# Kernel tuning notes

Hardware: AMD Instinct MI355X
Metric: run time of the kernel (lower is better)

## Reference

```python
import jax, jax.numpy as jnp
import numpy as np


def conv1x1(x, W, b):
    # x: [B,C,H,W], W: [O,C], b: [O]
    return jnp.einsum('bchw,oc->bohw', x, W) + b[None, :, None, None]


def setup_inputs() -> dict:
    key = jax.random.key(0)
    ks = jax.random.split(key, 16)
    B, C, H, W = 4, 256, 64, 64
    C4 = C // 4
    s = lambda fan_in: 1.0 / np.sqrt(fan_in)
    inp = {
        'last_frame': jax.random.normal(ks[0], (B, C, H, W), jnp.float32),
        'current_frame': jax.random.normal(ks[1], (B, C, H, W), jnp.float32),
        'future_frame': jax.random.normal(ks[2], (B, C, H, W), jnp.float32),
        'Wqk': jax.random.normal(ks[3], (C4, C), jnp.float32) * s(C),
        'bqk': jnp.zeros((C4,), jnp.float32),
        'Wkl': jax.random.normal(ks[4], (C4, C), jnp.float32) * s(C),
        'bkl': jnp.zeros((C4,), jnp.float32),
        'Wkf': jax.random.normal(ks[5], (C4, C), jnp.float32) * s(C),
        'bkf': jnp.zeros((C4,), jnp.float32),
        'Wv': jax.random.normal(ks[6], (C4, C), jnp.float32) * s(C),
        'bv': jnp.zeros((C4,), jnp.float32),
        'Wfire': jax.random.normal(ks[7], (C, C // 2), jnp.float32) * s(C // 2),
        'bfire': jnp.zeros((C,), jnp.float32),
        'bn_gamma': jnp.ones((C,), jnp.float32),
        'bn_beta': jnp.zeros((C,), jnp.float32),
        'bn_mean': jnp.zeros((C,), jnp.float32),
        'bn_var': jnp.ones((C,), jnp.float32),
    }
    return inp


def reference(last_frame, current_frame, future_frame,
              Wqk, bqk, Wkl, bkl, Wkf, bkf, Wv, bv,
              Wfire, bfire, bn_gamma, bn_beta, bn_mean, bn_var):
    B, C, H, W = current_frame.shape
    C4 = C // 4
    HW = H * W
    eps = 1e-5

    q = conv1x1(current_frame, Wqk, bqk).reshape(B, C4, HW)       # [B,C4,HW]
    kl = conv1x1(last_frame, Wkl, bkl).reshape(B, C4, HW)          # [B,C4,HW]
    kf = conv1x1(future_frame, Wkf, bkf).reshape(B, C4, HW)        # [B,C4,HW]
    v = conv1x1(current_frame, Wv, bv).reshape(B, C4, HW)          # [B,C4,HW]

    # affinity: [B, HW(query), HW(key)], softmax over key axis
    aff_l = jax.nn.softmax(jnp.einsum('bcq,bck->bqk', q, kl), axis=-1)
    aff_f = jax.nn.softmax(jnp.einsum('bcq,bck->bqk', q, kf), axis=-1)

    # out = V @ A^T : out[b,c,q] = sum_k v[b,c,k] * aff[b,q,k]
    out_l = jnp.einsum('bck,bqk->bcq', v, aff_l).reshape(B, C4, H, W)
    out_f = jnp.einsum('bck,bqk->bcq', v, aff_f).reshape(B, C4, H, W)

    fused = jnp.concatenate([out_l, out_f], axis=1)                 # [B,C/2,H,W]
    fired = conv1x1(fused, Wfire, bfire)                            # [B,C,H,W]
    # BatchNorm (inference form with running stats)
    inv = bn_gamma / jnp.sqrt(bn_var + eps)
    fired = fired * inv[None, :, None, None] + (bn_beta - bn_mean * inv)[None, :, None, None]
    return jax.nn.relu(current_frame + fired)
```

## Files before the change

### kernel.cpp

```cpp
#include <hip/hip_runtime.h>
#include <math.h>
#include <stdint.h>

#define HWN 4096
#define CIN 256
#define CQ 64
#define LOG2E 1.44269504f
#define C2OFF 56.0f

typedef __attribute__((ext_vector_type(8))) _Float16 f16x8;
typedef __attribute__((ext_vector_type(4))) _Float16 f16x4;
typedef __attribute__((ext_vector_type(8))) short    bf16x8;
typedef __attribute__((ext_vector_type(4))) short    bf16x4;
typedef __attribute__((ext_vector_type(4))) float    f32x4;

__device__ __forceinline__ short f2bf(float f) {
  union { float f; uint32_t u; } c; c.f = f;
  uint32_t r = (c.u + 0x7FFFu + ((c.u >> 16) & 1u)) >> 16;
  return (short)(uint16_t)r;
}

__device__ __forceinline__ void stage16(const void* g, void* l) {
  __builtin_amdgcn_global_load_lds(
      (const __attribute__((address_space(1))) uint32_t*)g,
      (__attribute__((address_space(3))) uint32_t*)l, 16, 0, 0);
}

__device__ __forceinline__ void pswap32(uint32_t& a, uint32_t& b) {
  asm volatile("v_permlane32_swap_b32 %0, %1" : "+v"(a), "+v"(b));
}
__device__ __forceinline__ void pswap16(uint32_t& a, uint32_t& b) {
  asm volatile("v_permlane16_swap_b32 %0, %1" : "+v"(a), "+v"(b));
}

__global__ __launch_bounds__(256) void prep_kernel(
    const float* __restrict__ Wqk, const float* __restrict__ Wkl,
    const float* __restrict__ Wkf, const float* __restrict__ Wv,
    const float* __restrict__ Wfire, const float* __restrict__ bfire,
    const float* __restrict__ gamma, const float* __restrict__ beta,
    const float* __restrict__ mean,  const float* __restrict__ var,
    _Float16* __restrict__ wqk_h, _Float16* __restrict__ wkl_h,
    _Float16* __restrict__ wkf_h, _Float16* __restrict__ wv_h,
    _Float16* __restrict__ wf_h, float* __restrict__ scale, float* __restrict__ shift) {
  int gid = blockIdx.x * 256 + threadIdx.x;
  if (gid < CQ * CIN) {
    wqk_h[gid] = (_Float16)(Wqk[gid] * LOG2E);
    wkl_h[gid] = (_Float16)Wkl[gid];
    wkf_h[gid] = (_Float16)Wkf[gid];
    wv_h[gid]  = (_Float16)Wv[gid];
  }
  if (gid < CIN * 128) wf_h[gid] = (_Float16)Wfire[gid];
  if (gid < CIN) {
    float inv = gamma[gid] / sqrtf(var[gid] + 1e-5f);
    scale[gid] = inv;
    shift[gid] = (bfire[gid] - mean[gid]) * inv + beta[gid];
  }
}

__global__ __launch_bounds__(256, 3) void proj_kernel(
    const float* __restrict__ cur, const float* __restrict__ last, const float* __restrict__ fut,
    const _Float16* __restrict__ wqk, const float* __restrict__ bqk,
    const _Float16* __restrict__ wkl, const float* __restrict__ bkl,
    const _Float16* __restrict__ wkf, const float* __restrict__ bkf,
    const _Float16* __restrict__ wv,  const float* __restrict__ bv,
    _Float16* __restrict__ q_out, _Float16* __restrict__ kl_out,
    _Float16* __restrict__ kf_out, short* __restrict__ v_out) {
  const int tid  = threadIdx.x;
  const int w    = tid >> 6;
  const int lane = tid & 63;
  const int quad = lane >> 4;
  const int l15  = lane & 15;
  const int pass = blockIdx.x >> 8;
  const int bb   = blockIdx.x & 255;
  const int b    = bb >> 6;
  const int hwt  = (bb & 63) << 6;
  const int hw   = hwt + w * 16 + l15;

  __shared__ __align__(16) float    Xs[2][8][260];
  __shared__ __align__(16) _Float16 Tl[4][16][72];

  const float* X = (pass == 0) ? cur : ((pass == 1) ? last : fut);
  const float* xb0 = X + (size_t)b * CIN * HWN + hwt;

  auto stageX = [&](int buf, int cc) {
#pragma unroll
    for (int i = 0; i < 2; ++i)
      stage16(xb0 + (size_t)(cc * 32 + w * 8 + i * 4 + (lane >> 3) / 2) * HWN +
                  ((lane & 15) << 2),
              &Xs[buf][w * 2 + i][0]);
  };

  const _Float16* W1 = (pass == 0) ? wqk : ((pass == 1) ? wkl : wkf);
  f32x4 a1[4] = {};
  f32x4 a2[4] = {};

  stageX(0, 0);
  __syncthreads();
#pragma unroll 1
  for (int cc = 0; cc < 8; ++cc) {
    const int buf = cc & 1;
    if (cc + 1 < 8) stageX(buf ^ 1, cc + 1);
    f16x8 bh;
#pragma unroll
    for (int j = 0; j < 8; ++j) {
      const int g = quad * 2 + (j >> 2);
      bh[j] = (_Float16)Xs[buf][g][(j & 3) * 64 + w * 16 + l15];
    }
#pragma unroll
    for (int mt = 0; mt < 4; ++mt) {
      f16x8 wa = *(const f16x8*)(W1 + (mt * 16 + l15) * CIN + cc * 32 + quad * 8);
      a1[mt] = __builtin_amdgcn_mfma_f32_16x16x32_f16(wa, bh, a1[mt], 0, 0, 0);
    }
    if (pass == 0) {
#pragma unroll
      for (int mt = 0; mt < 4; ++mt) {
        f16x8 wb = *(const f16x8*)(wv + (mt * 16 + l15) * CIN + cc * 32 + quad * 8);
        a2[mt] = __builtin_amdgcn_mfma_f32_16x16x32_f16(wb, bh, a2[mt], 0, 0, 0);
      }
    }
    __syncthreads();
  }

  if (pass == 0) {
#pragma unroll
    for (int mt = 0; mt < 4; ++mt)
#pragma unroll
      for (int r = 0; r < 4; ++r) {
        int oc = mt * 16 + quad * 4 + r;
        q_out[((size_t)b * CQ + oc) * HWN + hw] = (_Float16)(a1[mt][r] + bqk[oc] * LOG2E);
        v_out[((size_t)b * CQ + oc) * HWN + hw] = f2bf(a2[mt][r] + bv[oc]);
      }
  } else {
    const float* BI = (pass == 1) ? bkl : bkf;
    _Float16* OUT = (pass == 1) ? kl_out : kf_out;
#pragma unroll
    for (int mt = 0; mt < 4; ++mt) {
      f16x4 pw;
#pragma unroll
      for (int r = 0; r < 4; ++r)
        pw[r] = (_Float16)(a1[mt][r] + BI[mt * 16 + quad * 4 + r]);
      *(f16x4*)&Tl[w][l15][mt * 16 + quad * 4] = pw;
    }
#pragma unroll
    for (int kk = 0; kk < 2; ++kk) {
      f16x8 row = *(const f16x8*)&Tl[w][l15][kk * 32 + quad * 8];
      *(f16x8*)(OUT + ((size_t)b * HWN + hw) * CQ + kk * 32 + quad * 8) = row;
    }
  }
}

__global__ __launch_bounds__(256, 2) void attn_kernel(
    const _Float16* __restrict__ qbuf, const _Float16* __restrict__ klbuf,
    const _Float16* __restrict__ kfbuf, const short* __restrict__ vbuf,
    _Float16* __restrict__ fused) {
  const int tid  = threadIdx.x;
  const int w    = tid >> 6;
  const int lane = tid & 63;
  const int quad = lane >> 4;
  const int l15  = lane & 15;

  const int xcd  = blockIdx.x & 7;
  const int L    = xcd * 64 + (blockIdx.x >> 3);
  const int qt   = (L & 63) << 6;
  const int pair = (L >> 6) & 1;
  const int b    = L >> 7;

  const int kh = w >> 1;
  const int wq = w & 1;

  const _Float16* K  = (pair ? kfbuf : klbuf) + (size_t)b * HWN * CQ;
  const short*    Vg = vbuf + (size_t)b * CQ * HWN;

  __shared__ __align__(16) _Float16 Kt[2][2][64][64];
  __shared__ __align__(16) short    Vt[2][2][64][64];

  const int qbase = qt + wq * 32;
  f16x8 qfrag[2][2];
#pragma unroll
  for (int qg = 0; qg < 2; ++qg)
#pragma unroll
    for (int kk = 0; kk < 2; ++kk)
#pragma unroll
      for (int j = 0; j < 8; ++j)
        qfrag[qg][kk][j] = qbuf[(b * CQ + kk * 32 + quad * 8 + j) * HWN +
                                qbase + qg * 16 + l15];

  f32x4 Oacc[2][4] = {};
  float psum[2] = {0.f, 0.f};

  const int swz  = (lane & 7) ^ ((lane >> 3) & 7);
  const int rswz = l15 & 7;

  const _Float16* ksrc =
      K + ((size_t)(kh * 2048) + wq * 32 + (lane >> 3)) * CQ + swz * 8;
  const short* vsrcS =
      Vg + (size_t)(wq * 32 + (lane >> 3)) * HWN + kh * 2048 + swz * 8;

  auto stageK = [&](int buf, int t) {
#pragma unroll
    for (int r = 0; r < 4; ++r)
      stage16(ksrc + ((size_t)t * 64 + r * 8) * CQ,
              &Kt[buf][kh][wq * 32 + r * 8][0]);
  };
  auto stageV = [&](int buf, int t) {
#pragma unroll
    for (int r = 0; r < 4; ++r)
      stage16(vsrcS + (size_t)(r * 8) * HWN + t * 64,
              &Vt[buf][kh][wq * 32 + r * 8][0]);
  };

  auto body = [&](int buf) {
    f16x8 kf[4][2];
#pragma unroll
    for (int nt = 0; nt < 4; ++nt)
#pragma unroll
      for (int kk = 0; kk < 2; ++kk)
        kf[nt][kk] = *(const f16x8*)&Kt[buf][kh][nt * 16 + l15][((kk * 4 + quad) ^ rswz) * 8];
    bf16x8 vf[4][2];
#pragma unroll
    for (int ct = 0; ct < 4; ++ct)
#pragma unroll
      for (int kk = 0; kk < 2; ++kk)
        vf[ct][kk] = *(const bf16x8*)&Vt[buf][kh][ct * 16 + l15][((kk * 4 + quad) ^ rswz) * 8];
#pragma unroll
    for (int qg = 0; qg < 2; ++qg) {
      f32x4 ST[4] = {};
      __builtin_amdgcn_s_setprio(1);
#pragma unroll
      for (int nt = 0; nt < 4; ++nt)
#pragma unroll
        for (int kk = 0; kk < 2; ++kk)
          ST[nt] = __builtin_amdgcn_mfma_f32_16x16x32_f16(kf[nt][kk], qfrag[qg][kk],
                                                          ST[nt], 0, 0, 0);
      __builtin_amdgcn_s_setprio(0);
      uint32_t D[4][2];
#pragma unroll
      for (int nt = 0; nt < 4; ++nt)
#pragma unroll
        for (int e = 0; e < 2; ++e) {
          float p0 = __builtin_amdgcn_exp2f(ST[nt][2 * e]     - C2OFF);
          float p1 = __builtin_amdgcn_exp2f(ST[nt][2 * e + 1] - C2OFF);
          uint32_t u0 = __float_as_uint(p0) & 0xffff0000u;
          uint32_t u1 = __float_as_uint(p1) & 0xffff0000u;
          psum[qg] += __uint_as_float(u0) + __uint_as_float(u1);
          D[nt][e] = (u0 >> 16) | u1;
        }
#pragma unroll
      for (int kk = 0; kk < 2; ++kk) {
        uint32_t pa0, pa1, pa2, pa3;
        {
          uint32_t u = D[2 * kk][0], v = D[2 * kk + 1][0];
          pswap32(u, v); pswap16(u, v);
          pa0 = u; pa2 = v;
        }
        {
          uint32_t u = D[2 * kk][1], v = D[2 * kk + 1][1];
          pswap32(u, v); pswap16(u, v);
          pa1 = u; pa3 = v;
        }
        union { uint32_t u[4]; bf16x8 v8; } P;
        P.u[0] = pa0; P.u[1] = pa1; P.u[2] = pa2; P.u[3] = pa3;
        __builtin_amdgcn_s_setprio(1);
#pragma unroll
        for (int ct = 0; ct < 4; ++ct)
          Oacc[qg][ct] = __builtin_amdgcn_mfma_f32_16x16x32_bf16(P.v8, vf[ct][kk],
                                                                 Oacc[qg][ct], 0, 0, 0);
        __builtin_amdgcn_s_setprio(0);
      }
    }
  };

  stageK(0, 0); stageV(0, 0);
  __syncthreads();
#pragma unroll 1
  for (int tt = 0; tt < 32; tt += 2) {
    stageK(1, tt + 1); stageV(1, tt + 1);
    body(0);
    __syncthreads();
    if (tt + 2 < 32) { stageK(0, tt + 2); stageV(0, tt + 2); }
    body(1);
    __syncthreads();
  }

#pragma unroll
  for (int qg = 0; qg < 2; ++qg) {
    psum[qg] += __shfl_xor(psum[qg], 16);
    psum[qg] += __shfl_xor(psum[qg], 32);
  }

  float* sc = (float*)&Kt[0][0][0][0];
  float* sp = sc + 4096;
  if (kh) {
#pragma unroll
    for (int qg = 0; qg < 2; ++qg) {
#pragma unroll
      for (int ct = 0; ct < 4; ++ct)
        *(f32x4*)&sc[((((wq * 2 + qg) * 4) + ct) << 8) + lane * 4] = Oacc[qg][ct];
      sp[(wq * 2 + qg) * 64 + lane] = psum[qg];
    }
  }
  __syncthreads();
  if (!kh) {
#pragma unroll
    for (int qg = 0; qg < 2; ++qg) {
      psum[qg] += sp[(wq * 2 + qg) * 64 + lane];
#pragma unroll
      for (int ct = 0; ct < 4; ++ct) {
        f32x4 o2 = *(const f32x4*)&sc[((((wq * 2 + qg) * 4) + ct) << 8) + lane * 4];
        Oacc[qg][ct] += o2;
      }
#pragma unroll
      for (int r = 0; r < 4; ++r) {
        float lt = __shfl(psum[qg], quad * 4 + r);
        float invl = __builtin_amdgcn_rcpf(lt);
        int qi = qbase + qg * 16 + quad * 4 + r;
#pragma unroll
        for (int ct = 0; ct < 4; ++ct)
          fused[((size_t)b * HWN + qi) * 128 + pair * 64 + ct * 16 + l15] =
              (_Float16)(Oacc[qg][ct][r] * invl);
      }
    }
  }
}

__global__ __launch_bounds__(256) void fire_kernel(
    const _Float16* __restrict__ fused, const _Float16* __restrict__ wf,
    const float* __restrict__ scale, const float* __restrict__ shift,
    const float* __restrict__ cur, float* __restrict__ out) {
  const int tid  = threadIdx.x;
  const int w    = tid >> 6;
  const int lane = tid & 63;
  const int quad = lane >> 4;
  const int l15  = lane & 15;
  const int g    = blockIdx.x & 3;
  const int bb   = blockIdx.x >> 2;
  const int b    = bb >> 6;
  const int hwt  = (bb & 63) << 6;
  const int hwb  = hwt + w * 16;

  f16x8 bfr[4];
#pragma unroll
  for (int k0 = 0; k0 < 4; ++k0)
    bfr[k0] = *(const f16x8*)(fused + ((size_t)b * HWN + hwb + l15) * 128 + k0 * 32 + quad * 8);

  float curv[4][4];
#pragma unroll
  for (int mt = 0; mt < 4; ++mt)
#pragma unroll
    for (int r = 0; r < 4; ++r)
      curv[mt][r] = cur[((size_t)b * CIN + g * 64 + mt * 16 + quad * 4 + r) * HWN + hwb + l15];

  f32x4 acc[4] = {};
#pragma unroll
  for (int k0 = 0; k0 < 4; ++k0)
#pragma unroll
    for (int mt = 0; mt < 4; ++mt) {
      f16x8 af = *(const f16x8*)(wf + (g * 64 + mt * 16 + l15) * 128 + k0 * 32 + quad * 8);
      acc[mt] = __builtin_amdgcn_mfma_f32_16x16x32_f16(af, bfr[k0], acc[mt], 0, 0, 0);
    }

#pragma unroll
  for (int mt = 0; mt < 4; ++mt)
#pragma unroll
    for (int r = 0; r < 4; ++r) {
      int oc = g * 64 + mt * 16 + quad * 4 + r;
      size_t idx = ((size_t)b * CIN + oc) * HWN + hwb + l15;
      float y = curv[mt][r] + acc[mt][r] * scale[oc] + shift[oc];
      out[idx] = fmaxf(y, 0.f);
    }
}

extern "C" void kernel_launch(void* const* d_in, const int* in_sizes, int n_in,
                              void* d_out, int out_size, void* d_ws, size_t ws_size,
                              hipStream_t stream) {
  const float* last  = (const float*)d_in[0];
  const float* cur   = (const float*)d_in[1];
  const float* fut   = (const float*)d_in[2];
  const float* Wqk   = (const float*)d_in[3];
  const float* bqk   = (const float*)d_in[4];
  const float* Wkl   = (const float*)d_in[5];
  const float* bkl   = (const float*)d_in[6];
  const float* Wkf   = (const float*)d_in[7];
  const float* bkf   = (const float*)d_in[8];
  const float* Wv    = (const float*)d_in[9];
  const float* bv    = (const float*)d_in[10];
  const float* Wfire = (const float*)d_in[11];
  const float* bfire = (const float*)d_in[12];
  const float* gamma = (const float*)d_in[13];
  const float* beta  = (const float*)d_in[14];
  const float* mean  = (const float*)d_in[15];
  const float* var   = (const float*)d_in[16];

  char* ws = (char*)d_ws;
  _Float16* qb     = (_Float16*)(ws);
  _Float16* klb    = (_Float16*)(ws + (2u << 20));
  _Float16* kfb    = (_Float16*)(ws + (4u << 20));
  short*    vb     = (short*)   (ws + (6u << 20));
  _Float16* fusedb = (_Float16*)(ws + (8u << 20));
  char* wsm = ws + (12u << 20);
  _Float16* wqk_h = (_Float16*)(wsm);
  _Float16* wkl_h = (_Float16*)(wsm + (32u << 10));
  _Float16* wkf_h = (_Float16*)(wsm + (64u << 10));
  _Float16* wv_h  = (_Float16*)(wsm + (96u << 10));
  _Float16* wf_h  = (_Float16*)(wsm + (128u << 10));
  float*    scale = (float*)   (wsm + (192u << 10));
  float*    shift = (float*)   (wsm + (193u << 10));
  float*    out   = (float*)d_out;

  prep_kernel<<<128, 256, 0, stream>>>(Wqk, Wkl, Wkf, Wv, Wfire, bfire,
                                       gamma, beta, mean, var,
                                       wqk_h, wkl_h, wkf_h, wv_h, wf_h, scale, shift);
  proj_kernel<<<768, 256, 0, stream>>>(cur, last, fut, wqk_h, bqk, wkl_h, bkl,
                                       wkf_h, bkf, wv_h, bv, qb, klb, kfb, vb);
  attn_kernel<<<512, 256, 0, stream>>>(qb, klb, kfb, vb, fusedb);
  fire_kernel<<<1024, 256, 0, stream>>>(fusedb, wf_h, scale, shift, cur, out);
}
```

Measured before the change: 194.9 us.

## Compute softmax row sums via MFMA with ones vector and packed bf16 convert

Replaces per-element bf16 truncation and scalar accumulation of the softmax denominator with a hardware packed f32-to-bf16 conversion, and computes row sums by an extra MFMA of P against a vector of ones. This removes VALU adds and the cross-lane shuffles at the end, at the cost of one more MFMA per kk step and round-to-nearest instead of truncation. The fire kernel also remaps block indices so that consecutive logical tiles land on the same XCD, for better L2 locality.

```diff
diff --git a/kernel.cpp b/kernel.cpp
--- a/kernel.cpp
+++ b/kernel.cpp
@@ -186,7 +186,11 @@
                                 qbase + qg * 16 + l15];
 
   f32x4 Oacc[2][4] = {};
-  float psum[2] = {0.f, 0.f};
+  f32x4 Osum[2]    = {};
+
+  bf16x8 vones;
+#pragma unroll
+  for (int j = 0; j < 8; ++j) vones[j] = (short)0x3F80;
 
   const int swz  = (lane & 7) ^ ((lane >> 3) & 7);
   const int rswz = l15 & 7;
@@ -240,10 +244,8 @@
         for (int e = 0; e < 2; ++e) {
           float p0 = __builtin_amdgcn_exp2f(ST[nt][2 * e]     - C2OFF);
           float p1 = __builtin_amdgcn_exp2f(ST[nt][2 * e + 1] - C2OFF);
-          uint32_t u0 = __float_as_uint(p0) & 0xffff0000u;
-          uint32_t u1 = __float_as_uint(p1) & 0xffff0000u;
-          psum[qg] += __uint_as_float(u0) + __uint_as_float(u1);
-          D[nt][e] = (u0 >> 16) | u1;
+          asm("v_cvt_pk_bf16_f32 %0, %1, %2"
+              : "=v"(D[nt][e]) : "v"(p0), "v"(p1));
         }
 #pragma unroll
       for (int kk = 0; kk < 2; ++kk) {
@@ -265,6 +267,8 @@
         for (int ct = 0; ct < 4; ++ct)
           Oacc[qg][ct] = __builtin_amdgcn_mfma_f32_16x16x32_bf16(P.v8, vf[ct][kk],
                                                                  Oacc[qg][ct], 0, 0, 0);
+        Osum[qg] = __builtin_amdgcn_mfma_f32_16x16x32_bf16(P.v8, vones,
+                                                           Osum[qg], 0, 0, 0);
         __builtin_amdgcn_s_setprio(0);
       }
     }
@@ -282,28 +286,22 @@
     __syncthreads();
   }
 
-#pragma unroll
-  for (int qg = 0; qg < 2; ++qg) {
-    psum[qg] += __shfl_xor(psum[qg], 16);
-    psum[qg] += __shfl_xor(psum[qg], 32);
-  }
-
   float* sc = (float*)&Kt[0][0][0][0];
-  float* sp = sc + 4096;
+  f32x4* sv = (f32x4*)(sc + 4096);
   if (kh) {
 #pragma unroll
     for (int qg = 0; qg < 2; ++qg) {
 #pragma unroll
       for (int ct = 0; ct < 4; ++ct)
         *(f32x4*)&sc[((((wq * 2 + qg) * 4) + ct) << 8) + lane * 4] = Oacc[qg][ct];
-      sp[(wq * 2 + qg) * 64 + lane] = psum[qg];
+      sv[(wq * 2 + qg) * 64 + lane] = Osum[qg];
     }
   }
   __syncthreads();
   if (!kh) {
 #pragma unroll
     for (int qg = 0; qg < 2; ++qg) {
-      psum[qg] += sp[(wq * 2 + qg) * 64 + lane];
+      Osum[qg] += sv[(wq * 2 + qg) * 64 + lane];
 #pragma unroll
       for (int ct = 0; ct < 4; ++ct) {
         f32x4 o2 = *(const f32x4*)&sc[((((wq * 2 + qg) * 4) + ct) << 8) + lane * 4];
@@ -311,8 +309,7 @@
       }
 #pragma unroll
       for (int r = 0; r < 4; ++r) {
-        float lt = __shfl(psum[qg], quad * 4 + r);
-        float invl = __builtin_amdgcn_rcpf(lt);
+        float invl = __builtin_amdgcn_rcpf(Osum[qg][r]);
         int qi = qbase + qg * 16 + quad * 4 + r;
 #pragma unroll
         for (int ct = 0; ct < 4; ++ct)
@@ -332,8 +329,10 @@
   const int lane = tid & 63;
   const int quad = lane >> 4;
   const int l15  = lane & 15;
-  const int g    = blockIdx.x & 3;
-  const int bb   = blockIdx.x >> 2;
+  const int xcd  = blockIdx.x & 7;
+  const int Lf   = xcd * 128 + (blockIdx.x >> 3);
+  const int g    = Lf & 3;
+  const int bb   = Lf >> 2;
   const int b    = bb >> 6;
   const int hwt  = (bb & 63) << 6;
   const int hwb  = hwt + w * 16;
```

After: 193.6 us. About the same (-0.7%).
